# Kernel optimization log

Hardware: AMD Instinct MI355X
Metric: run time of the kernel (lower is better)

The kernel has to match this reference:

```python
import jax, jax.numpy as jnp
import numpy as np

# Sparse MinkUNet-style backbone sizes
N0, N1, N2, N3 = 100000, 50000, 25000, 12500  # voxels per level (batch-concatenated)
K, KD = 27, 8        # 3x3x3 kernel offsets, stride-2 child offsets
B, S = 8, 1024       # batch, seed_num
C0, C1, C2, C3 = 32, 64, 128, 256
COUT = 512


def _w(k, shape, fan_in):
    return jax.random.normal(k, shape, dtype=jnp.float32) / np.sqrt(fan_in)


def setup_inputs() -> dict:
    key = jax.random.key(0)
    ks = jax.random.split(key, 32)
    inp = {}
    inp["feats"] = jax.random.normal(ks[0], (N0, 3), dtype=jnp.float32)
    # neighbor maps (kernel-offset gather indices, as built by a voxel hash map)
    inp["nbr0"] = jax.random.randint(ks[1], (N0, K), 0, N0, dtype=jnp.int32)
    inp["nbr1"] = jax.random.randint(ks[2], (N1, K), 0, N1, dtype=jnp.int32)
    inp["nbr2"] = jax.random.randint(ks[3], (N2, K), 0, N2, dtype=jnp.int32)
    inp["nbr3"] = jax.random.randint(ks[4], (N3, K), 0, N3, dtype=jnp.int32)
    # stride-2 downsample maps (coarse voxel -> fine children)
    inp["down1"] = jax.random.randint(ks[5], (N1, KD), 0, N0, dtype=jnp.int32)
    inp["down2"] = jax.random.randint(ks[6], (N2, KD), 0, N1, dtype=jnp.int32)
    inp["down3"] = jax.random.randint(ks[7], (N3, KD), 0, N2, dtype=jnp.int32)
    # nearest-parent upsample maps (fine voxel -> coarse parent)
    inp["up2"] = jax.random.randint(ks[8], (N2,), 0, N3, dtype=jnp.int32)
    inp["up1"] = jax.random.randint(ks[9], (N1,), 0, N2, dtype=jnp.int32)
    inp["up0"] = jax.random.randint(ks[10], (N0,), 0, N1, dtype=jnp.int32)
    # nearest-voxel devoxelize index for each FPS seed point
    inp["seed_idx"] = jax.random.randint(ks[11], (B, S), 0, N0, dtype=jnp.int32)
    # conv kernels [K, Cin, Cout] and 1x1 (linear) decoder weights
    inp["W_stem"] = _w(ks[12], (K, 3, C0), K * 3)
    inp["W_b0"] = _w(ks[13], (K, C0, C0), K * C0)
    inp["W_d1"] = _w(ks[14], (KD, C0, C1), KD * C0)
    inp["W_b1"] = _w(ks[15], (K, C1, C1), K * C1)
    inp["W_d2"] = _w(ks[16], (KD, C1, C2), KD * C1)
    inp["W_b2"] = _w(ks[17], (K, C2, C2), K * C2)
    inp["W_d3"] = _w(ks[18], (KD, C2, C3), KD * C2)
    inp["W_b3"] = _w(ks[19], (K, C3, C3), K * C3)
    inp["W_u2"] = _w(ks[20], (C3 + C2, 256), C3 + C2)
    inp["W_u1"] = _w(ks[21], (256 + C1, 128), 256 + C1)
    inp["W_u0"] = _w(ks[22], (128 + C0, 96), 128 + C0)
    inp["W_out"] = _w(ks[23], (96, COUT), 96)
    return inp


def sp_conv(f, nbr, W):
    # gather neighbor features then contract over (kernel offset, in-channel)
    g = f[nbr]                                # [N, K, Cin]
    return jnp.einsum('nkc,kco->no', g, W)    # [N, Cout]


def reference(feats, nbr0, nbr1, nbr2, nbr3, down1, down2, down3,
              up2, up1, up0, seed_idx,
              W_stem, W_b0, W_d1, W_b1, W_d2, W_b2, W_d3, W_b3,
              W_u2, W_u1, W_u0, W_out):
    relu = jax.nn.relu
    # encoder
    x0 = relu(sp_conv(feats, nbr0, W_stem))          # [N0, 32]
    x0 = x0 + relu(sp_conv(x0, nbr0, W_b0))
    x1 = relu(sp_conv(x0, down1, W_d1))              # [N1, 64]
    x1 = x1 + relu(sp_conv(x1, nbr1, W_b1))
    x2 = relu(sp_conv(x1, down2, W_d2))              # [N2, 128]
    x2 = x2 + relu(sp_conv(x2, nbr2, W_b2))
    x3 = relu(sp_conv(x2, down3, W_d3))              # [N3, 256]
    x3 = x3 + relu(sp_conv(x3, nbr3, W_b3))
    # decoder: nearest-parent upsample + skip concat + 1x1 conv
    u2 = relu(jnp.concatenate([x3[up2], x2], axis=-1) @ W_u2)   # [N2, 256]
    u1 = relu(jnp.concatenate([u2[up1], x1], axis=-1) @ W_u1)   # [N1, 128]
    u0 = relu(jnp.concatenate([u1[up0], x0], axis=-1) @ W_u0)   # [N0, 96]
    out_vox = u0 @ W_out                                        # [N0, 512]
    seed_feats = out_vox[seed_idx]                              # [B, S, 512]
    return jnp.transpose(seed_feats, (0, 2, 1))                 # [B, 512, S]
```

## Files before the change

kernel.cpp:

```cpp
#include <hip/hip_runtime.h>

typedef unsigned short u16;
typedef unsigned int u32;
typedef __bf16 bf16x8 __attribute__((ext_vector_type(8)));
typedef float f32x4 __attribute__((ext_vector_type(4)));

#define NV0 100000
#define NV1 50000
#define NV2 25000
#define NV3 12500

enum : long {
  OFF_WB0  = 0,
  OFF_WD1  = 27648,
  OFF_WB1  = 44032,
  OFF_WD2  = 154624,
  OFF_WB2  = 220160,
  OFF_WD3  = 662528,
  OFF_WB3  = 924672,
  OFF_WU2  = 2694144,
  OFF_WU1  = 2792448,
  OFF_WU0  = 2833408,
  OFF_WOUT = 2848768,
  OFF_TA   = 2897920,
  OFF_X0   = OFF_TA  + 3200000,
  OFF_X1   = OFF_X0  + 3200000,
  OFF_X2   = OFF_X1  + 3200000,
  OFF_X3   = OFF_X2  + 3200000,
  OFF_U2   = OFF_X3  + 3200000,
  OFF_U1   = OFF_U2  + 6400000,
  OFF_U0S  = OFF_U1  + 6400000,
  OFF_END  = OFF_U0S + 786432,
};

__device__ __forceinline__ float b2f(u16 u) {
  union { u32 i; float f; } x; x.i = ((u32)u) << 16; return x.f;
}
__device__ __forceinline__ u16 f2b(float f) {
  union { float f; u32 i; } x; x.f = f;
  u32 r = (x.i + 0x7FFFu + ((x.i >> 16) & 1u)) >> 16;
  return (u16)r;
}
__device__ __forceinline__ void gload16(const u16* g, const u16* l) {
  __builtin_amdgcn_global_load_lds(
      (const __attribute__((address_space(1))) void*)g,
      (__attribute__((address_space(3))) void*)(u16*)l, 16, 0, 0);
}
__device__ __forceinline__ void store_out(u16* p, float v)  { *p = f2b(v); }
__device__ __forceinline__ void store_out(float* p, float v) { *p = v; }
constexpr int ilog2c(int x) { return x <= 1 ? 0 : 1 + ilog2c(x / 2); }

struct PD { const float* src; u16* dst; int KK, CIN, COUT; };
struct PrepArgs { PD d[11]; };

__global__ __launch_bounds__(256) void prep_k(PrepArgs pa) {
  const PD d = pa.d[blockIdx.y];
  const int cc = d.CIN * d.COUT;
  const int total = d.KK * cc;
  for (int e = blockIdx.x * 256 + threadIdx.x; e < total; e += gridDim.x * 256) {
    int k = e / cc;
    int r = e - k * cc;
    int c = r / d.COUT;
    int o = r - c * d.COUT;
    d.dst[(k * d.COUT + o) * d.CIN + c] = f2b(d.src[e]);
  }
}

__global__ __launch_bounds__(256) void stem_k(const float* __restrict__ feats,
                                              const int* __restrict__ nbr0,
                                              const float* __restrict__ wstem,
                                              u16* __restrict__ out) {
  __shared__ float Wl[27 * 3 * 32];
  const int tid = threadIdx.x;
  for (int i = tid; i < 2592; i += 256) Wl[i] = wstem[i];
  __syncthreads();
  const int n = blockIdx.x * 8 + (tid >> 5);
  const int o = tid & 31;
  if (n >= NV0) return;
  float acc = 0.f;
  const int* nb = nbr0 + n * 27;
  #pragma unroll
  for (int k = 0; k < 27; k++) {
    const int iv = nb[k];
    const float* f = feats + iv * 3;
    acc = fmaf(f[0], Wl[(k * 3 + 0) * 32 + o], acc);
    acc = fmaf(f[1], Wl[(k * 3 + 1) * 32 + o], acc);
    acc = fmaf(f[2], Wl[(k * 3 + 2) * 32 + o], acc);
  }
  out[n * 32 + o] = f2b(fmaxf(acc, 0.f));
}

template <int BM, int BN, int WM, int WN, int COUTF, int KCT, int BK, int MODE,
          int CIN, int KK, int CA, bool RES, bool DORELU, typename OT>
__global__ __launch_bounds__(256, 4) void gemm_k(
    const u16* __restrict__ src0, const u16* __restrict__ src1,
    const int* __restrict__ idx0, const int* __restrict__ idx1,
    const u16* __restrict__ wt, const u16* __restrict__ base,
    OT* __restrict__ out, int N) {
  constexpr int NWM = BM / WM, NWN = BN / WN;
  static_assert(NWM * NWN == 4, "4 waves");
  constexpr int MI = WM / 16, NI = WN / 16;
  constexpr int CB = KCT - CA;
  constexpr int SLOTS = BK / 8;
  constexpr int SM = SLOTS - 1;
  constexpr int LSL = ilog2c(SLOTS);
  constexpr int RPC = 64 / SLOTS;
  constexpr int LRPC = ilog2c(RPC);
  constexpr int ACH = (BM * BK) / 512;
  constexpr int BCH = (BN * BK) / 512;
  constexpr int NIT = KCT / BK;
  constexpr int LOGC = ilog2c(CIN);
  constexpr int NIDX = (MODE == 0) ? BM * KK : (MODE == 1 ? BM : (MODE == 2 ? 2 * BM : 1));
  static_assert(KCT % BK == 0, "K mult of BK");
  static_assert(MODE != 1 || (CA % BK == 0), "concat boundary aligned");

  __shared__ u16 As[2][BM * BK];
  __shared__ u16 Bs[2][BN * BK];
  __shared__ int Is[NIDX];
  const int tid = threadIdx.x;
  const int w = tid >> 6, lane = tid & 63;
  const int quad = lane >> 4, l16 = lane & 15;
  const int wm = w % NWM, wn = w / NWM;
  const int row0 = blockIdx.x * BM;
  const int col0 = blockIdx.y * BN;
  const int Nm1 = N - 1;
  const int srow = lane >> LSL;
  const int g    = (lane & SM) ^ (srow & SM);
  const int cl   = g * 8;

  if constexpr (MODE == 0) {
    for (int e = tid; e < BM * KK; e += 256) {
      const int r = e / KK, k = e - r * KK;
      int n = row0 + r; n = (n > Nm1) ? Nm1 : n;
      Is[e] = idx0[(long)n * KK + k];
    }
  } else if constexpr (MODE == 1) {
    for (int e = tid; e < BM; e += 256) {
      int n = row0 + e; n = (n > Nm1) ? Nm1 : n;
      Is[e] = idx0[n];
    }
  } else if constexpr (MODE == 2) {
    for (int e = tid; e < BM; e += 256) {
      int n = row0 + e; n = (n > Nm1) ? Nm1 : n;
      const int s = idx0[n];
      Is[e] = idx1[s];
      Is[BM + e] = s;
    }
  }
  if constexpr (MODE != 3) __syncthreads();

  f32x4 acc[MI][NI];
  #pragma unroll
  for (int i = 0; i < MI; i++)
    #pragma unroll
    for (int j = 0; j < NI; j++) acc[i][j] = {0.f, 0.f, 0.f, 0.f};

  auto stage = [&](int buf, int kc0) {
    for (int c = w; c < ACH + BCH; c += 4) {
      const int cab = kc0 + cl;
      if (c < ACH) {
        const int r = (c << LRPC) + srow;
        const u16* gp;
        if constexpr (MODE == 0) {
          const int k = cab >> LOGC;
          gp = src0 + (long)Is[r * KK + k] * CIN + (cab & (CIN - 1));
        } else if constexpr (MODE == 1) {
          if (kc0 < CA) gp = src0 + (long)Is[r] * CA + cab;
          else {
            int n = row0 + r; n = (n > Nm1) ? Nm1 : n;
            gp = src1 + (long)n * CB + (cab - CA);
          }
        } else if constexpr (MODE == 2) {
          if (kc0 < CA) gp = src0 + (long)Is[r] * CA + cab;
          else          gp = src1 + (long)Is[BM + r] * CB + (cab - CA);
        } else {
          int n = row0 + r; n = (n > Nm1) ? Nm1 : n;
          gp = src0 + (long)n * KCT + cab;
        }
        gload16(gp, &As[buf][c * 512]);
      } else {
        const int cb = c - ACH;
        const int o = col0 + (cb << LRPC) + srow;
        const u16* gp;
        if constexpr (MODE == 0) {
          const int k = cab >> LOGC;
          gp = wt + ((long)(k * COUTF + o)) * CIN + (cab & (CIN - 1));
        } else {
          gp = wt + (long)o * KCT + cab;
        }
        gload16(gp, &Bs[buf][cb * 512]);
      }
    }
  };

  stage(0, 0);
  #pragma unroll 1
  for (int it = 0; it < NIT; it++) {
    __syncthreads();
    if (it + 1 < NIT) stage((it + 1) & 1, (it + 1) * BK);
    const int buf = it & 1;
    #pragma unroll
    for (int kk = 0; kk < BK / 32; kk++) {
      bf16x8 af[MI], bfr[NI];
      #pragma unroll
      for (int i = 0; i < MI; i++) {
        const int row = wm * WM + i * 16 + l16;
        const int slot = row * SLOTS + (((kk << 2) + quad) ^ (row & SM));
        af[i] = *(const bf16x8*)&As[buf][slot * 8];
      }
      #pragma unroll
      for (int j = 0; j < NI; j++) {
        const int row = wn * WN + j * 16 + l16;
        const int slot = row * SLOTS + (((kk << 2) + quad) ^ (row & SM));
        bfr[j] = *(const bf16x8*)&Bs[buf][slot * 8];
      }
      #pragma unroll
      for (int i = 0; i < MI; i++)
        #pragma unroll
        for (int j = 0; j < NI; j++)
          acc[i][j] = __builtin_amdgcn_mfma_f32_16x16x32_bf16(af[i], bfr[j], acc[i][j], 0, 0, 0);
    }
  }

  #pragma unroll
  for (int i = 0; i < MI; i++) {
    #pragma unroll
    for (int j = 0; j < NI; j++) {
      const int col = col0 + wn * WN + j * 16 + l16;
      #pragma unroll
      for (int r = 0; r < 4; r++) {
        const int n = row0 + wm * WM + i * 16 + quad * 4 + r;
        if (n < N) {
          float v = acc[i][j][r];
          if constexpr (RES)         v = b2f(base[(long)n * COUTF + col]) + fmaxf(v, 0.f);
          else if constexpr (DORELU) v = fmaxf(v, 0.f);
          store_out(&out[(long)n * COUTF + col], v);
        }
      }
    }
  }
}

__global__ __launch_bounds__(256) void tout_k(const float* __restrict__ tmp,
                                              float* __restrict__ outp) {
  __shared__ float tl[64][65];
  const int tid = threadIdx.x;
  const int r0 = blockIdx.x * 64, o0 = blockIdx.y * 64;
  {
    const int rl = tid >> 2, oc = (tid & 3) * 16;
    const float* src = &tmp[(r0 + rl) * 512 + o0 + oc];
    #pragma unroll
    for (int j = 0; j < 16; j++) tl[rl][oc + j] = src[j];
  }
  __syncthreads();
  {
    const int ol = tid >> 2, sc = (tid & 3) * 16;
    const int b = r0 >> 10, s0 = r0 & 1023;
    float* dst = &outp[((long)b * 512 + (o0 + ol)) * 1024 + s0 + sc];
    #pragma unroll
    for (int j = 0; j < 16; j++) dst[j] = tl[sc + j][ol];
  }
}

extern "C" void kernel_launch(void* const* d_in, const int* in_sizes, int n_in,
                              void* d_out, int out_size, void* d_ws, size_t ws_size,
                              hipStream_t stream) {
  const float* feats = (const float*)d_in[0];
  const int* nbr0  = (const int*)d_in[1];
  const int* nbr1  = (const int*)d_in[2];
  const int* nbr2  = (const int*)d_in[3];
  const int* nbr3  = (const int*)d_in[4];
  const int* down1 = (const int*)d_in[5];
  const int* down2 = (const int*)d_in[6];
  const int* down3 = (const int*)d_in[7];
  const int* up2   = (const int*)d_in[8];
  const int* up1   = (const int*)d_in[9];
  const int* up0   = (const int*)d_in[10];
  const int* seed  = (const int*)d_in[11];
  u16* ws = (u16*)d_ws;

  PrepArgs pa;
  pa.d[0]  = {(const float*)d_in[13], ws + OFF_WB0,  27, 32, 32};
  pa.d[1]  = {(const float*)d_in[14], ws + OFF_WD1,  8,  32, 64};
  pa.d[2]  = {(const float*)d_in[15], ws + OFF_WB1,  27, 64, 64};
  pa.d[3]  = {(const float*)d_in[16], ws + OFF_WD2,  8,  64, 128};
  pa.d[4]  = {(const float*)d_in[17], ws + OFF_WB2,  27, 128, 128};
  pa.d[5]  = {(const float*)d_in[18], ws + OFF_WD3,  8,  128, 256};
  pa.d[6]  = {(const float*)d_in[19], ws + OFF_WB3,  27, 256, 256};
  pa.d[7]  = {(const float*)d_in[20], ws + OFF_WU2,  1,  384, 256};
  pa.d[8]  = {(const float*)d_in[21], ws + OFF_WU1,  1,  320, 128};
  pa.d[9]  = {(const float*)d_in[22], ws + OFF_WU0,  1,  160, 96};
  pa.d[10] = {(const float*)d_in[23], ws + OFF_WOUT, 1,  96,  512};
  prep_k<<<dim3(128, 11), 256, 0, stream>>>(pa);

  u16* ta  = ws + OFF_TA;
  u16* x0  = ws + OFF_X0;
  u16* x1  = ws + OFF_X1;
  u16* x2  = ws + OFF_X2;
  u16* x3  = ws + OFF_X3;
  u16* u2b = ws + OFF_U2;
  u16* u1b = ws + OFF_U1;
  u16* u0s = ws + OFF_U0S;
  float* tmp = (float*)(ws + OFF_TA);

  stem_k<<<12500, 256, 0, stream>>>(feats, nbr0, (const float*)d_in[12], ta);

  gemm_k<128, 32, 32, 32, 32, 864, 32, 0, 32, 27, 0, true, true, u16>
      <<<dim3(782, 1), 256, 0, stream>>>(ta, nullptr, nbr0, nullptr, ws + OFF_WB0, ta, x0, NV0);
  gemm_k<64, 64, 32, 32, 64, 256, 64, 0, 32, 8, 0, false, true, u16>
      <<<dim3(782, 1), 256, 0, stream>>>(x0, nullptr, down1, nullptr, ws + OFF_WD1, nullptr, ta, NV1);
  gemm_k<64, 64, 32, 32, 64, 1728, 64, 0, 64, 27, 0, true, true, u16>
      <<<dim3(782, 1), 256, 0, stream>>>(ta, nullptr, nbr1, nullptr, ws + OFF_WB1, ta, x1, NV1);
  gemm_k<64, 64, 32, 32, 128, 512, 64, 0, 64, 8, 0, false, true, u16>
      <<<dim3(391, 2), 256, 0, stream>>>(x1, nullptr, down2, nullptr, ws + OFF_WD2, nullptr, ta, NV2);
  gemm_k<64, 64, 32, 32, 128, 3456, 64, 0, 128, 27, 0, true, true, u16>
      <<<dim3(391, 2), 256, 0, stream>>>(ta, nullptr, nbr2, nullptr, ws + OFF_WB2, ta, x2, NV2);
  gemm_k<64, 64, 32, 32, 256, 1024, 64, 0, 128, 8, 0, false, true, u16>
      <<<dim3(196, 4), 256, 0, stream>>>(x2, nullptr, down3, nullptr, ws + OFF_WD3, nullptr, ta, NV3);
  gemm_k<64, 64, 32, 32, 256, 6912, 64, 0, 256, 27, 0, true, true, u16>
      <<<dim3(196, 4), 256, 0, stream>>>(ta, nullptr, nbr3, nullptr, ws + OFF_WB3, ta, x3, NV3);
  gemm_k<64, 64, 32, 32, 256, 384, 64, 1, 32, 1, 256, false, true, u16>
      <<<dim3(391, 4), 256, 0, stream>>>(x3, x2, up2, nullptr, ws + OFF_WU2, nullptr, u2b, NV2);
  gemm_k<64, 64, 32, 32, 128, 320, 64, 1, 32, 1, 256, false, true, u16>
      <<<dim3(782, 2), 256, 0, stream>>>(u2b, x1, up1, nullptr, ws + OFF_WU1, nullptr, u1b, NV1);
  gemm_k<64, 96, 32, 48, 96, 160, 32, 2, 32, 1, 128, false, true, u16>
      <<<dim3(128, 1), 256, 0, stream>>>(u1b, x0, seed, up0, ws + OFF_WU0, nullptr, u0s, 8192);
  gemm_k<64, 64, 32, 32, 512, 96, 32, 3, 32, 1, 0, false, false, float>
      <<<dim3(128, 8), 256, 0, stream>>>(u0s, nullptr, nullptr, nullptr, ws + OFF_WOUT, nullptr, tmp, 8192);
  tout_k<<<dim3(128, 8), 256, 0, stream>>>(tmp, (float*)d_out);
}
```

Baseline: 527.7 us.

## Split-K the deep sparse convs over kernel offsets and enlarge GEMM tiles

Adds a split-K mode for the gather GEMM: the 27 kernel offsets are split across blockIdx.z. Each split writes fp32 partial sums, and a new combine kernel adds the partials, applies ReLU and adds the residual. Most of the other GEMM launches get larger tiles (128-row or 128-column) so that more output columns share each gathered A row. The goal is better parallelism on the small coarse levels and better reuse elsewhere. The cost is extra fp32 partial traffic, an added kernel launch, and lower occupancy from the larger tiles (min waves set to 2).

```diff
diff --git a/kernel.cpp b/kernel.cpp
--- a/kernel.cpp
+++ b/kernel.cpp
@@ -4,6 +4,7 @@
 typedef unsigned int u32;
 typedef __bf16 bf16x8 __attribute__((ext_vector_type(8)));
 typedef float f32x4 __attribute__((ext_vector_type(4)));
+typedef u16 u16x4 __attribute__((ext_vector_type(4)));
 
 #define NV0 100000
 #define NV1 50000
@@ -91,8 +92,9 @@
 }
 
 template <int BM, int BN, int WM, int WN, int COUTF, int KCT, int BK, int MODE,
-          int CIN, int KK, int CA, bool RES, bool DORELU, typename OT>
-__global__ __launch_bounds__(256, 4) void gemm_k(
+          int CIN, int KK, int KSP, int CA, bool RES, bool DORELU, bool PARTIAL,
+          int MINW, typename OT>
+__global__ __launch_bounds__(256, MINW) void gemm_k(
     const u16* __restrict__ src0, const u16* __restrict__ src1,
     const int* __restrict__ idx0, const int* __restrict__ idx1,
     const u16* __restrict__ wt, const u16* __restrict__ base,
@@ -108,9 +110,9 @@
   constexpr int LRPC = ilog2c(RPC);
   constexpr int ACH = (BM * BK) / 512;
   constexpr int BCH = (BN * BK) / 512;
-  constexpr int NIT = KCT / BK;
   constexpr int LOGC = ilog2c(CIN);
-  constexpr int NIDX = (MODE == 0) ? BM * KK : (MODE == 1 ? BM : (MODE == 2 ? 2 * BM : 1));
+  constexpr int LBM = ilog2c(BM);
+  constexpr int NIDX = (MODE == 0) ? BM * KSP : (MODE == 1 ? BM : (MODE == 2 ? 2 * BM : 1));
   static_assert(KCT % BK == 0, "K mult of BK");
   static_assert(MODE != 1 || (CA % BK == 0), "concat boundary aligned");
 
@@ -124,15 +126,21 @@
   const int row0 = blockIdx.x * BM;
   const int col0 = blockIdx.y * BN;
   const int Nm1 = N - 1;
+  const int k0 = (MODE == 0) ? (int)blockIdx.z * KSP : 0;
+  const int k1 = (MODE == 0) ? ((k0 + KSP > KK) ? KK : k0 + KSP) : 0;
+  const int kcb = (MODE == 0) ? k0 * CIN : 0;
+  const int kce = (MODE == 0) ? k1 * CIN : KCT;
+  if constexpr (PARTIAL) out += (long)blockIdx.z * N * COUTF;
   const int srow = lane >> LSL;
   const int g    = (lane & SM) ^ (srow & SM);
   const int cl   = g * 8;
 
   if constexpr (MODE == 0) {
-    for (int e = tid; e < BM * KK; e += 256) {
-      const int r = e / KK, k = e - r * KK;
+    const int kcnt = k1 - k0;
+    for (int e = tid; e < kcnt * BM; e += 256) {
+      const int kl = e >> LBM, r = e & (BM - 1);
       int n = row0 + r; n = (n > Nm1) ? Nm1 : n;
-      Is[e] = idx0[(long)n * KK + k];
+      Is[e] = idx0[(long)n * KK + k0 + kl];
     }
   } else if constexpr (MODE == 1) {
     for (int e = tid; e < BM; e += 256) {
@@ -163,7 +171,7 @@
         const u16* gp;
         if constexpr (MODE == 0) {
           const int k = cab >> LOGC;
-          gp = src0 + (long)Is[r * KK + k] * CIN + (cab & (CIN - 1));
+          gp = src0 + (long)Is[((k - k0) << LBM) | r] * CIN + (cab & (CIN - 1));
         } else if constexpr (MODE == 1) {
           if (kc0 < CA) gp = src0 + (long)Is[r] * CA + cab;
           else {
@@ -193,11 +201,12 @@
     }
   };
 
-  stage(0, 0);
+  const int nit = (kce - kcb) / BK;
+  stage(0, kcb);
   #pragma unroll 1
-  for (int it = 0; it < NIT; it++) {
+  for (int it = 0; it < nit; it++) {
     __syncthreads();
-    if (it + 1 < NIT) stage((it + 1) & 1, (it + 1) * BK);
+    if (it + 1 < nit) stage((it + 1) & 1, kcb + (it + 1) * BK);
     const int buf = it & 1;
     #pragma unroll
     for (int kk = 0; kk < BK / 32; kk++) {
@@ -241,6 +250,20 @@
   }
 }
 
+__global__ __launch_bounds__(256) void comb_k(const float* __restrict__ P,
+                                              const u16* __restrict__ base,
+                                              u16* __restrict__ out, int total) {
+  const int i = (blockIdx.x * 256 + threadIdx.x) * 4;
+  if (i >= total) return;
+  const f32x4 a = *(const f32x4*)&P[i];
+  const f32x4 b = *(const f32x4*)&P[total + i];
+  u16x4 o;
+  #pragma unroll
+  for (int j = 0; j < 4; j++)
+    o[j] = f2b(b2f(base[i + j]) + fmaxf(a[j] + b[j], 0.f));
+  *(u16x4*)&out[i] = o;
+}
+
 __global__ __launch_bounds__(256) void tout_k(const float* __restrict__ tmp,
                                               float* __restrict__ outp) {
   __shared__ float tl[64][65];
@@ -301,31 +324,34 @@
   u16* u2b = ws + OFF_U2;
   u16* u1b = ws + OFF_U1;
   u16* u0s = ws + OFF_U0S;
+  float* P   = (float*)(ws + OFF_U2);
   float* tmp = (float*)(ws + OFF_TA);
 
   stem_k<<<12500, 256, 0, stream>>>(feats, nbr0, (const float*)d_in[12], ta);
 
-  gemm_k<128, 32, 32, 32, 32, 864, 32, 0, 32, 27, 0, true, true, u16>
-      <<<dim3(782, 1), 256, 0, stream>>>(ta, nullptr, nbr0, nullptr, ws + OFF_WB0, ta, x0, NV0);
-  gemm_k<64, 64, 32, 32, 64, 256, 64, 0, 32, 8, 0, false, true, u16>
-      <<<dim3(782, 1), 256, 0, stream>>>(x0, nullptr, down1, nullptr, ws + OFF_WD1, nullptr, ta, NV1);
-  gemm_k<64, 64, 32, 32, 64, 1728, 64, 0, 64, 27, 0, true, true, u16>
-      <<<dim3(782, 1), 256, 0, stream>>>(ta, nullptr, nbr1, nullptr, ws + OFF_WB1, ta, x1, NV1);
-  gemm_k<64, 64, 32, 32, 128, 512, 64, 0, 64, 8, 0, false, true, u16>
-      <<<dim3(391, 2), 256, 0, stream>>>(x1, nullptr, down2, nullptr, ws + OFF_WD2, nullptr, ta, NV2);
-  gemm_k<64, 64, 32, 32, 128, 3456, 64, 0, 128, 27, 0, true, true, u16>
-      <<<dim3(391, 2), 256, 0, stream>>>(ta, nullptr, nbr2, nullptr, ws + OFF_WB2, ta, x2, NV2);
-  gemm_k<64, 64, 32, 32, 256, 1024, 64, 0, 128, 8, 0, false, true, u16>
-      <<<dim3(196, 4), 256, 0, stream>>>(x2, nullptr, down3, nullptr, ws + OFF_WD3, nullptr, ta, NV3);
-  gemm_k<64, 64, 32, 32, 256, 6912, 64, 0, 256, 27, 0, true, true, u16>
-      <<<dim3(196, 4), 256, 0, stream>>>(ta, nullptr, nbr3, nullptr, ws + OFF_WB3, ta, x3, NV3);
-  gemm_k<64, 64, 32, 32, 256, 384, 64, 1, 32, 1, 256, false, true, u16>
-      <<<dim3(391, 4), 256, 0, stream>>>(x3, x2, up2, nullptr, ws + OFF_WU2, nullptr, u2b, NV2);
-  gemm_k<64, 64, 32, 32, 128, 320, 64, 1, 32, 1, 256, false, true, u16>
-      <<<dim3(782, 2), 256, 0, stream>>>(u2b, x1, up1, nullptr, ws + OFF_WU1, nullptr, u1b, NV1);
-  gemm_k<64, 96, 32, 48, 96, 160, 32, 2, 32, 1, 128, false, true, u16>
-      <<<dim3(128, 1), 256, 0, stream>>>(u1b, x0, seed, up0, ws + OFF_WU0, nullptr, u0s, 8192);
-  gemm_k<64, 64, 32, 32, 512, 96, 32, 3, 32, 1, 0, false, false, float>
-      <<<dim3(128, 8), 256, 0, stream>>>(u0s, nullptr, nullptr, nullptr, ws + OFF_WOUT, nullptr, tmp, 8192);
+  gemm_k<128, 32, 32, 32, 32, 864, 32, 0, 32, 27, 27, 0, true, true, false, 4, u16>
+      <<<dim3(782, 1, 1), 256, 0, stream>>>(ta, nullptr, nbr0, nullptr, ws + OFF_WB0, ta, x0, NV0);
+  gemm_k<128, 64, 64, 32, 64, 256, 64, 0, 32, 8, 8, 0, false, true, false, 4, u16>
+      <<<dim3(391, 1, 1), 256, 0, stream>>>(x0, nullptr, down1, nullptr, ws + OFF_WD1, nullptr, ta, NV1);
+  gemm_k<128, 64, 64, 32, 64, 1728, 32, 0, 64, 27, 27, 0, true, true, false, 4, u16>
+      <<<dim3(391, 1, 1), 256, 0, stream>>>(ta, nullptr, nbr1, nullptr, ws + OFF_WB1, ta, x1, NV1);
+  gemm_k<64, 128, 32, 64, 128, 512, 64, 0, 64, 8, 8, 0, false, true, false, 4, u16>
+      <<<dim3(391, 1, 1), 256, 0, stream>>>(x1, nullptr, down2, nullptr, ws + OFF_WD2, nullptr, ta, NV2);
+  gemm_k<128, 128, 64, 64, 128, 3456, 32, 0, 128, 27, 14, 0, false, false, true, 2, float>
+      <<<dim3(196, 1, 2), 256, 0, stream>>>(ta, nullptr, nbr2, nullptr, ws + OFF_WB2, nullptr, P, NV2);
+  comb_k<<<dim3(3125), 256, 0, stream>>>(P, ta, x2, NV2 * 128);
+  gemm_k<64, 128, 32, 64, 256, 1024, 64, 0, 128, 8, 8, 0, false, true, false, 4, u16>
+      <<<dim3(196, 2, 1), 256, 0, stream>>>(x2, nullptr, down3, nullptr, ws + OFF_WD3, nullptr, ta, NV3);
+  gemm_k<128, 128, 64, 64, 256, 6912, 32, 0, 256, 27, 14, 0, false, false, true, 2, float>
+      <<<dim3(98, 2, 2), 256, 0, stream>>>(ta, nullptr, nbr3, nullptr, ws + OFF_WB3, nullptr, P, NV3);
+  comb_k<<<dim3(3125), 256, 0, stream>>>(P, ta, x3, NV3 * 256);
+  gemm_k<64, 128, 32, 64, 256, 384, 64, 1, 32, 1, 1, 256, false, true, false, 4, u16>
+      <<<dim3(391, 2, 1), 256, 0, stream>>>(x3, x2, up2, nullptr, ws + OFF_WU2, nullptr, u2b, NV2);
+  gemm_k<64, 128, 32, 64, 128, 320, 64, 1, 32, 1, 1, 256, false, true, false, 4, u16>
+      <<<dim3(782, 1, 1), 256, 0, stream>>>(u2b, x1, up1, nullptr, ws + OFF_WU1, nullptr, u1b, NV1);
+  gemm_k<64, 96, 32, 48, 96, 160, 32, 2, 32, 1, 1, 128, false, true, false, 4, u16>
+      <<<dim3(128, 1, 1), 256, 0, stream>>>(u1b, x0, seed, up0, ws + OFF_WU0, nullptr, u0s, 8192);
+  gemm_k<64, 128, 32, 64, 512, 96, 32, 3, 32, 1, 1, 0, false, false, false, 4, float>
+      <<<dim3(128, 4, 1), 256, 0, stream>>>(u0s, nullptr, nullptr, nullptr, ws + OFF_WOUT, nullptr, tmp, 8192);
   tout_k<<<dim3(128, 8), 256, 0, stream>>>(tmp, (float*)d_out);
 }
```

Result: slower. 540.5 us (+2.4%).
